# Kernel tuning notes

Measured on AMD Instinct MI355X. Metric: run time of the kernel, lower is better.

Reference implementation:

```python
import jax, jax.numpy as jnp
import numpy as np

N = 8192
D = 256
ALPHA = 0.2  # LeakyReLU negative slope
NEG_INF = -9e15


def setup_inputs() -> dict:
    key = jax.random.key(0)
    k1, k2, k3, k4, k5, k6 = jax.random.split(key, 6)
    inputs = jax.random.normal(k1, (N, D), dtype=jnp.float32)
    # sparse random binary adjacency, avg degree ~32, plus self loops
    adj = (jax.random.uniform(k2, (N, N)) < (32.0 / N)).astype(jnp.float32)
    adj = jnp.maximum(adj, jnp.eye(N, dtype=jnp.float32))
    cmt_weight = jax.random.uniform(k3, (N, 1), dtype=jnp.float32)  # unused by SPGAT
    W = jax.random.normal(k4, (D, D), dtype=jnp.float32) * (1.0 / np.sqrt(D))
    a1 = jax.random.normal(k5, (D, 1), dtype=jnp.float32) * 0.1
    a2 = jax.random.normal(k6, (D, 1), dtype=jnp.float32) * 0.1
    return {"inputs": inputs, "adj": adj, "cmt_weight": cmt_weight,
            "W": W, "a1": a1, "a2": a2}


def reference(inputs, adj, cmt_weight, W, a1, a2):
    # SPGAT (batched GAT layer with batch=1, squeezed):
    Wh = inputs @ W                       # [N, D]
    f1 = Wh @ a1                          # [N, 1]
    f2 = Wh @ a2                          # [N, 1]
    e = jax.nn.leaky_relu(f1 + f2.T, negative_slope=ALPHA)  # [N, N]
    scores = jnp.where(adj > 0, e, NEG_INF)
    att = jax.nn.softmax(scores, axis=-1)  # [N, N]
    node_out = jax.nn.relu(att @ Wh)       # [N, D]
    return node_out
```

## Files before the change

### kernel.cpp

```cpp
#include <hip/hip_runtime.h>
#include <hip/hip_bf16.h>
#include <math.h>

#define NN 8192
#define DD 256
#define DEG_CAP 128
constexpr float ALPHA = 0.2f;

typedef __attribute__((ext_vector_type(4))) float f32x4;
typedef __attribute__((ext_vector_type(8))) short bf16x8;
typedef __attribute__((ext_vector_type(8))) unsigned short u16x8;

__global__ __launch_bounds__(256) void k_convX(const float* __restrict__ X,
                                               short* __restrict__ Xhi,
                                               short* __restrict__ Xlo) {
    int i = blockIdx.x * 256 + threadIdx.x;
    float4 v = ((const float4*)X)[i];
    float f[4] = {v.x, v.y, v.z, v.w};
    short h[4], l[4];
    #pragma unroll
    for (int q = 0; q < 4; ++q) {
        __hip_bfloat16 hb = __float2bfloat16(f[q]);
        float hf = __bfloat162float(hb);
        __hip_bfloat16 lb = __float2bfloat16(f[q] - hf);
        h[q] = __builtin_bit_cast(short, hb);
        l[q] = __builtin_bit_cast(short, lb);
    }
    *(short4*)(Xhi + (size_t)i * 4) = make_short4(h[0], h[1], h[2], h[3]);
    *(short4*)(Xlo + (size_t)i * 4) = make_short4(l[0], l[1], l[2], l[3]);
}

__global__ __launch_bounds__(256) void k_convW(const float* __restrict__ W,
                                               short* __restrict__ WhiT,
                                               short* __restrict__ WloT) {
    __shared__ float tile[64][65];
    const int n0 = (blockIdx.x & 3) * 64;
    const int k0 = (blockIdx.x >> 2) * 64;
    const int c = threadIdx.x & 63;
    const int rg = threadIdx.x >> 6;
    #pragma unroll
    for (int i = 0; i < 16; ++i) {
        int r = rg * 16 + i;
        tile[r][c] = W[(size_t)(k0 + r) * DD + n0 + c];
    }
    __syncthreads();
    #pragma unroll
    for (int i = 0; i < 16; ++i) {
        int rw = rg * 16 + i;
        float x = tile[c][rw];
        __hip_bfloat16 hb = __float2bfloat16(x);
        float hf = __bfloat162float(hb);
        __hip_bfloat16 lb = __float2bfloat16(x - hf);
        WhiT[(size_t)(n0 + rw) * DD + k0 + c] = __builtin_bit_cast(short, hb);
        WloT[(size_t)(n0 + rw) * DD + k0 + c] = __builtin_bit_cast(short, lb);
    }
}

#define LDA 40
__global__ __launch_bounds__(256) void k_gemm(const short* __restrict__ Xhi,
                                              const short* __restrict__ Xlo,
                                              const short* __restrict__ WhiT,
                                              const short* __restrict__ WloT,
                                              float* __restrict__ Wh,
                                              unsigned short* __restrict__ Whb) {
    __shared__ short sAh[64 * LDA], sAl[64 * LDA];
    __shared__ short sBh[64 * LDA], sBl[64 * LDA];
    const int tid = threadIdx.x;
    const int lane = tid & 63;
    const int wid = tid >> 6;
    const int wm = wid >> 1, wn = wid & 1;
    const int row0 = (blockIdx.x >> 2) * 64;
    const int col0 = (blockIdx.x & 3) * 64;
    f32x4 acc[2][2] = {};
    for (int k0 = 0; k0 < DD; k0 += 32) {
        {
            int r = tid >> 2, sg = tid & 3;
            *(int4*)(sAh + r * LDA + sg * 8) =
                *(const int4*)(Xhi + (size_t)(row0 + r) * DD + k0 + sg * 8);
            *(int4*)(sAl + r * LDA + sg * 8) =
                *(const int4*)(Xlo + (size_t)(row0 + r) * DD + k0 + sg * 8);
            *(int4*)(sBh + r * LDA + sg * 8) =
                *(const int4*)(WhiT + (size_t)(col0 + r) * DD + k0 + sg * 8);
            *(int4*)(sBl + r * LDA + sg * 8) =
                *(const int4*)(WloT + (size_t)(col0 + r) * DD + k0 + sg * 8);
        }
        __syncthreads();
        const int kb = (lane >> 4) * 8;
        const int ar = wm * 32 + (lane & 15);
        const int br = wn * 32 + (lane & 15);
        bf16x8 ah[2], al[2], bh[2], bl[2];
        #pragma unroll
        for (int mi = 0; mi < 2; ++mi) {
            ah[mi] = *(const bf16x8*)(sAh + (ar + mi * 16) * LDA + kb);
            al[mi] = *(const bf16x8*)(sAl + (ar + mi * 16) * LDA + kb);
        }
        #pragma unroll
        for (int ni = 0; ni < 2; ++ni) {
            bh[ni] = *(const bf16x8*)(sBh + (br + ni * 16) * LDA + kb);
            bl[ni] = *(const bf16x8*)(sBl + (br + ni * 16) * LDA + kb);
        }
        #pragma unroll
        for (int mi = 0; mi < 2; ++mi)
            #pragma unroll
            for (int ni = 0; ni < 2; ++ni) {
                acc[mi][ni] = __builtin_amdgcn_mfma_f32_16x16x32_bf16(ah[mi], bh[ni], acc[mi][ni], 0, 0, 0);
                acc[mi][ni] = __builtin_amdgcn_mfma_f32_16x16x32_bf16(ah[mi], bl[ni], acc[mi][ni], 0, 0, 0);
                acc[mi][ni] = __builtin_amdgcn_mfma_f32_16x16x32_bf16(al[mi], bh[ni], acc[mi][ni], 0, 0, 0);
            }
        __syncthreads();
    }
    const int orow = row0 + wm * 32 + (lane >> 4) * 4;
    const int ocol = col0 + wn * 32 + (lane & 15);
    #pragma unroll
    for (int mi = 0; mi < 2; ++mi)
        #pragma unroll
        for (int ni = 0; ni < 2; ++ni)
            #pragma unroll
            for (int r = 0; r < 4; ++r) {
                float x = acc[mi][ni][r];
                size_t idx = (size_t)(orow + mi * 16 + r) * DD + ocol + ni * 16;
                Wh[idx] = x;
                Whb[idx] = __builtin_bit_cast(unsigned short, __float2bfloat16(x));
            }
}

__global__ __launch_bounds__(256) void k_f12(const float* __restrict__ Wh,
                                             const float* __restrict__ a1,
                                             const float* __restrict__ a2,
                                             float* __restrict__ f1,
                                             float* __restrict__ f2) {
    const int wid = threadIdx.x >> 6;
    const int lane = threadIdx.x & 63;
    const int row = blockIdx.x * 4 + wid;
    float4 w  = *(const float4*)(Wh + (size_t)row * DD + lane * 4);
    float4 v1 = *(const float4*)(a1 + lane * 4);
    float4 v2 = *(const float4*)(a2 + lane * 4);
    float s1 = w.x * v1.x + w.y * v1.y + w.z * v1.z + w.w * v1.w;
    float s2 = w.x * v2.x + w.y * v2.y + w.z * v2.z + w.w * v2.w;
    #pragma unroll
    for (int o = 32; o; o >>= 1) {
        s1 += __shfl_down(s1, o);
        s2 += __shfl_down(s2, o);
    }
    if (lane == 0) { f1[row] = s1; f2[row] = s2; }
}

__global__ __launch_bounds__(256) void k_gat6(const float* __restrict__ adj,
                                              const unsigned short* __restrict__ Whb,
                                              const float* __restrict__ f1,
                                              const float* __restrict__ f2,
                                              float* __restrict__ out) {
    __shared__ int   s_j[4][DEG_CAP];
    __shared__ float s_e[4][DEG_CAP];
    const int tid = threadIdx.x;
    const int lane = tid & 63, wid = tid >> 6;
    const int row = blockIdx.x * 4 + wid;
    s_e[wid][lane]      = -INFINITY;
    s_e[wid][lane + 64] = -INFINITY;
    const float f1i = f1[row];
    const f32x4* arow = (const f32x4*)(adj + (size_t)row * NN);
    int base = 0;
    for (int ch = 0; ch < 8; ++ch) {
        f32x4 v[4];
        #pragma unroll
        for (int u = 0; u < 4; ++u)
            v[u] = __builtin_nontemporal_load(&arow[ch * 256 + u * 64 + lane]);
        #pragma unroll
        for (int u = 0; u < 4; ++u) {
            #pragma unroll
            for (int q = 0; q < 4; ++q) {
                bool hit = v[u][q] > 0.f;
                unsigned long long mask = __ballot(hit);
                if (hit) {
                    int pos = base + __popcll(mask & ((1ull << lane) - 1ull));
                    if (pos < DEG_CAP) {
                        int j = (ch * 256 + u * 64 + lane) * 4 + q;
                        float e = f1i + f2[j];
                        e = e > 0.f ? e : ALPHA * e;
                        s_j[wid][pos] = j;
                        s_e[wid][pos] = e;
                    }
                }
                base += __popcll(mask);
            }
        }
    }
    const int cw = base < DEG_CAP ? base : DEG_CAP;
    float e0 = s_e[wid][lane], e1 = s_e[wid][lane + 64];
    float mx = fmaxf(e0, e1);
    #pragma unroll
    for (int o = 32; o; o >>= 1) mx = fmaxf(mx, __shfl_xor(mx, o));
    float sm = __expf(e0 - mx) + __expf(e1 - mx);
    #pragma unroll
    for (int o = 32; o; o >>= 1) sm += __shfl_xor(sm, o);
    const int half = lane >> 5, sl = lane & 31;
    const int* sj = s_j[wid];
    const float* se = s_e[wid];
    f32x4 accA = {0.f, 0.f, 0.f, 0.f};
    f32x4 accB = {0.f, 0.f, 0.f, 0.f};
    {
        auto ld = [&](int kk) -> u16x8 {
            int idx = kk + half;
            int j = sj[idx < cw ? idx : 0];
            return *(const u16x8*)(Whb + (size_t)j * DD + sl * 8);
        };
        u16x8 b0 = ld(0), b1 = ld(2), b2 = ld(4), b3 = ld(6);
        for (int kk = 0; kk < cw; kk += 8) {
            #pragma unroll
            for (int p = 0; p < 4; ++p) {
                u16x8 cur = p == 0 ? b0 : p == 1 ? b1 : p == 2 ? b2 : b3;
                int idx = kk + p * 2 + half;
                float w = idx < cw ? __expf(se[idx] - mx) : 0.f;
                #pragma unroll
                for (int q = 0; q < 4; ++q) {
                    float lo = __builtin_bit_cast(float, (unsigned)cur[2 * q] << 16);
                    float hi = __builtin_bit_cast(float, (unsigned)cur[2 * q + 1] << 16);
                    if (q < 2) {
                        accA[2 * q]     = fmaf(w, lo, accA[2 * q]);
                        accA[2 * q + 1] = fmaf(w, hi, accA[2 * q + 1]);
                    } else {
                        accB[2 * (q - 2)]     = fmaf(w, lo, accB[2 * (q - 2)]);
                        accB[2 * (q - 2) + 1] = fmaf(w, hi, accB[2 * (q - 2) + 1]);
                    }
                }
            }
            b0 = ld(kk + 8); b1 = ld(kk + 10); b2 = ld(kk + 12); b3 = ld(kk + 14);
        }
    }
    #pragma unroll
    for (int q = 0; q < 4; ++q) {
        accA[q] += __shfl_xor(accA[q], 32);
        accB[q] += __shfl_xor(accB[q], 32);
    }
    const float inv = 1.f / sm;
    if (half == 0) {
        f32x4 r0, r1;
        #pragma unroll
        for (int q = 0; q < 4; ++q) {
            float oa = accA[q] * inv, ob = accB[q] * inv;
            r0[q] = oa > 0.f ? oa : 0.f;
            r1[q] = ob > 0.f ? ob : 0.f;
        }
        float* op = out + (size_t)row * DD + sl * 8;
        __builtin_nontemporal_store(r0, (f32x4*)op);
        __builtin_nontemporal_store(r1, (f32x4*)(op + 4));
    }
}

extern "C" void kernel_launch(void* const* d_in, const int* in_sizes, int n_in,
                              void* d_out, int out_size, void* d_ws, size_t ws_size,
                              hipStream_t stream) {
    const float* X   = (const float*)d_in[0];
    const float* adj = (const float*)d_in[1];
    const float* W   = (const float*)d_in[3];
    const float* a1  = (const float*)d_in[4];
    const float* a2  = (const float*)d_in[5];
    float* out = (float*)d_out;

    short* Xhi  = (short*)d_ws;
    short* Xlo  = Xhi + (size_t)NN * DD;
    short* WhiT = Xlo + (size_t)NN * DD;
    short* WloT = WhiT + (size_t)DD * DD;
    float* Wh   = (float*)(WloT + (size_t)DD * DD);
    float* f1   = Wh + (size_t)NN * DD;
    float* f2   = f1 + NN;
    unsigned short* Whb = (unsigned short*)(f2 + NN);

    k_convX<<<(NN * DD / 4) / 256, 256, 0, stream>>>(X, Xhi, Xlo);
    k_convW<<<16, 256, 0, stream>>>(W, WhiT, WloT);
    k_gemm<<<(NN / 64) * (DD / 64), 256, 0, stream>>>(Xhi, Xlo, WhiT, WloT, Wh, Whb);
    k_f12<<<NN / 4, 256, 0, stream>>>(Wh, a1, a2, f1, f2);
    k_gat6<<<NN / 4, 256, 0, stream>>>(adj, Whb, f1, f2, out);
}
```

Before: 82.94 us.

## Fuse X split conversion and f1/f2 projection into a full-width GEMM

Removes the separate X hi/lo conversion kernel and the f1/f2 dot-product kernel. The GEMM now reads fp32 X directly, splits it to bf16 hi/lo in shared memory, and computes a full 256-column row tile per block so it can reduce Wh·a1 and Wh·a2 in the epilogue. It no longer writes the fp32 Wh buffer. This cuts global traffic and launches, but each block now reloads the whole W^T slice per k-step and uses more LDS, which may lower occupancy.

```diff
diff --git a/kernel.cpp b/kernel.cpp
--- a/kernel.cpp
+++ b/kernel.cpp
@@ -10,25 +10,6 @@
 typedef __attribute__((ext_vector_type(4))) float f32x4;
 typedef __attribute__((ext_vector_type(8))) short bf16x8;
 typedef __attribute__((ext_vector_type(8))) unsigned short u16x8;
-
-__global__ __launch_bounds__(256) void k_convX(const float* __restrict__ X,
-                                               short* __restrict__ Xhi,
-                                               short* __restrict__ Xlo) {
-    int i = blockIdx.x * 256 + threadIdx.x;
-    float4 v = ((const float4*)X)[i];
-    float f[4] = {v.x, v.y, v.z, v.w};
-    short h[4], l[4];
-    #pragma unroll
-    for (int q = 0; q < 4; ++q) {
-        __hip_bfloat16 hb = __float2bfloat16(f[q]);
-        float hf = __bfloat162float(hb);
-        __hip_bfloat16 lb = __float2bfloat16(f[q] - hf);
-        h[q] = __builtin_bit_cast(short, hb);
-        l[q] = __builtin_bit_cast(short, lb);
-    }
-    *(short4*)(Xhi + (size_t)i * 4) = make_short4(h[0], h[1], h[2], h[3]);
-    *(short4*)(Xlo + (size_t)i * 4) = make_short4(l[0], l[1], l[2], l[3]);
-}
 
 __global__ __launch_bounds__(256) void k_convW(const float* __restrict__ W,
                                                short* __restrict__ WhiT,
@@ -56,93 +37,103 @@
     }
 }
 
-#define LDA 40
-__global__ __launch_bounds__(256) void k_gemm(const short* __restrict__ Xhi,
-                                              const short* __restrict__ Xlo,
-                                              const short* __restrict__ WhiT,
-                                              const short* __restrict__ WloT,
-                                              float* __restrict__ Wh,
-                                              unsigned short* __restrict__ Whb) {
-    __shared__ short sAh[64 * LDA], sAl[64 * LDA];
-    __shared__ short sBh[64 * LDA], sBl[64 * LDA];
+#define LDAx 40
+__global__ __launch_bounds__(256) void k_gemm2(const float* __restrict__ X,
+                                               const short* __restrict__ WhiT,
+                                               const short* __restrict__ WloT,
+                                               const float* __restrict__ a1,
+                                               const float* __restrict__ a2,
+                                               unsigned short* __restrict__ Whb,
+                                               float* __restrict__ f1,
+                                               float* __restrict__ f2) {
+    __shared__ short sAh[32 * LDAx], sAl[32 * LDAx];
+    __shared__ short sBh[256 * LDAx], sBl[256 * LDAx];
+    __shared__ float sP[2][2][32];
     const int tid = threadIdx.x;
     const int lane = tid & 63;
     const int wid = tid >> 6;
     const int wm = wid >> 1, wn = wid & 1;
-    const int row0 = (blockIdx.x >> 2) * 64;
-    const int col0 = (blockIdx.x & 3) * 64;
-    f32x4 acc[2][2] = {};
+    const int row0 = blockIdx.x * 32;
+    f32x4 acc[4][2] = {};
     for (int k0 = 0; k0 < DD; k0 += 32) {
         {
-            int r = tid >> 2, sg = tid & 3;
-            *(int4*)(sAh + r * LDA + sg * 8) =
-                *(const int4*)(Xhi + (size_t)(row0 + r) * DD + k0 + sg * 8);
-            *(int4*)(sAl + r * LDA + sg * 8) =
-                *(const int4*)(Xlo + (size_t)(row0 + r) * DD + k0 + sg * 8);
-            *(int4*)(sBh + r * LDA + sg * 8) =
-                *(const int4*)(WhiT + (size_t)(col0 + r) * DD + k0 + sg * 8);
-            *(int4*)(sBl + r * LDA + sg * 8) =
-                *(const int4*)(WloT + (size_t)(col0 + r) * DD + k0 + sg * 8);
+            int r = tid >> 3, c4 = tid & 7;
+            f32x4 xv = *(const f32x4*)(X + (size_t)(row0 + r) * DD + k0 + c4 * 4);
+            short hx[4], lx[4];
+            #pragma unroll
+            for (int q = 0; q < 4; ++q) {
+                __hip_bfloat16 hb = __float2bfloat16(xv[q]);
+                float hf = __bfloat162float(hb);
+                __hip_bfloat16 lb = __float2bfloat16(xv[q] - hf);
+                hx[q] = __builtin_bit_cast(short, hb);
+                lx[q] = __builtin_bit_cast(short, lb);
+            }
+            *(short4*)(sAh + r * LDAx + c4 * 4) = make_short4(hx[0], hx[1], hx[2], hx[3]);
+            *(short4*)(sAl + r * LDAx + c4 * 4) = make_short4(lx[0], lx[1], lx[2], lx[3]);
+            const int4* srcH = (const int4*)(WhiT + (size_t)tid * DD + k0);
+            const int4* srcL = (const int4*)(WloT + (size_t)tid * DD + k0);
+            #pragma unroll
+            for (int j = 0; j < 4; ++j) {
+                *(int4*)(sBh + tid * LDAx + j * 8) = srcH[j];
+                *(int4*)(sBl + tid * LDAx + j * 8) = srcL[j];
+            }
         }
         __syncthreads();
         const int kb = (lane >> 4) * 8;
-        const int ar = wm * 32 + (lane & 15);
-        const int br = wn * 32 + (lane & 15);
-        bf16x8 ah[2], al[2], bh[2], bl[2];
-        #pragma unroll
-        for (int mi = 0; mi < 2; ++mi) {
-            ah[mi] = *(const bf16x8*)(sAh + (ar + mi * 16) * LDA + kb);
-            al[mi] = *(const bf16x8*)(sAl + (ar + mi * 16) * LDA + kb);
-        }
+        const int l15 = lane & 15;
+        bf16x8 ah = *(const bf16x8*)(sAh + (wm * 16 + l15) * LDAx + kb);
+        bf16x8 al = *(const bf16x8*)(sAl + (wm * 16 + l15) * LDAx + kb);
+        #pragma unroll
+        for (int ct = 0; ct < 4; ++ct)
+            #pragma unroll
+            for (int ni = 0; ni < 2; ++ni) {
+                int br = ct * 64 + wn * 32 + ni * 16 + l15;
+                bf16x8 bh = *(const bf16x8*)(sBh + br * LDAx + kb);
+                bf16x8 bl = *(const bf16x8*)(sBl + br * LDAx + kb);
+                acc[ct][ni] = __builtin_amdgcn_mfma_f32_16x16x32_bf16(ah, bh, acc[ct][ni], 0, 0, 0);
+                acc[ct][ni] = __builtin_amdgcn_mfma_f32_16x16x32_bf16(ah, bl, acc[ct][ni], 0, 0, 0);
+                acc[ct][ni] = __builtin_amdgcn_mfma_f32_16x16x32_bf16(al, bh, acc[ct][ni], 0, 0, 0);
+            }
+        __syncthreads();
+    }
+    const int l15 = lane & 15;
+    const int orow = row0 + wm * 16 + (lane >> 4) * 4;
+    float s1[4] = {0.f, 0.f, 0.f, 0.f}, s2[4] = {0.f, 0.f, 0.f, 0.f};
+    #pragma unroll
+    for (int ct = 0; ct < 4; ++ct)
         #pragma unroll
         for (int ni = 0; ni < 2; ++ni) {
-            bh[ni] = *(const bf16x8*)(sBh + (br + ni * 16) * LDA + kb);
-            bl[ni] = *(const bf16x8*)(sBl + (br + ni * 16) * LDA + kb);
-        }
-        #pragma unroll
-        for (int mi = 0; mi < 2; ++mi)
-            #pragma unroll
-            for (int ni = 0; ni < 2; ++ni) {
-                acc[mi][ni] = __builtin_amdgcn_mfma_f32_16x16x32_bf16(ah[mi], bh[ni], acc[mi][ni], 0, 0, 0);
-                acc[mi][ni] = __builtin_amdgcn_mfma_f32_16x16x32_bf16(ah[mi], bl[ni], acc[mi][ni], 0, 0, 0);
-                acc[mi][ni] = __builtin_amdgcn_mfma_f32_16x16x32_bf16(al[mi], bh[ni], acc[mi][ni], 0, 0, 0);
-            }
-        __syncthreads();
-    }
-    const int orow = row0 + wm * 32 + (lane >> 4) * 4;
-    const int ocol = col0 + wn * 32 + (lane & 15);
-    #pragma unroll
-    for (int mi = 0; mi < 2; ++mi)
-        #pragma unroll
-        for (int ni = 0; ni < 2; ++ni)
+            int cc = ct * 64 + wn * 32 + ni * 16 + l15;
+            float A1 = a1[cc], A2 = a2[cc];
             #pragma unroll
             for (int r = 0; r < 4; ++r) {
-                float x = acc[mi][ni][r];
-                size_t idx = (size_t)(orow + mi * 16 + r) * DD + ocol + ni * 16;
-                Wh[idx] = x;
-                Whb[idx] = __builtin_bit_cast(unsigned short, __float2bfloat16(x));
-            }
-}
-
-__global__ __launch_bounds__(256) void k_f12(const float* __restrict__ Wh,
-                                             const float* __restrict__ a1,
-                                             const float* __restrict__ a2,
-                                             float* __restrict__ f1,
-                                             float* __restrict__ f2) {
-    const int wid = threadIdx.x >> 6;
-    const int lane = threadIdx.x & 63;
-    const int row = blockIdx.x * 4 + wid;
-    float4 w  = *(const float4*)(Wh + (size_t)row * DD + lane * 4);
-    float4 v1 = *(const float4*)(a1 + lane * 4);
-    float4 v2 = *(const float4*)(a2 + lane * 4);
-    float s1 = w.x * v1.x + w.y * v1.y + w.z * v1.z + w.w * v1.w;
-    float s2 = w.x * v2.x + w.y * v2.y + w.z * v2.z + w.w * v2.w;
-    #pragma unroll
-    for (int o = 32; o; o >>= 1) {
-        s1 += __shfl_down(s1, o);
-        s2 += __shfl_down(s2, o);
-    }
-    if (lane == 0) { f1[row] = s1; f2[row] = s2; }
+                float x = acc[ct][ni][r];
+                Whb[(size_t)(orow + r) * DD + cc] =
+                    __builtin_bit_cast(unsigned short, __float2bfloat16(x));
+                s1[r] = fmaf(x, A1, s1[r]);
+                s2[r] = fmaf(x, A2, s2[r]);
+            }
+        }
+    #pragma unroll
+    for (int o = 1; o < 16; o <<= 1)
+        #pragma unroll
+        for (int r = 0; r < 4; ++r) {
+            s1[r] += __shfl_xor(s1[r], o);
+            s2[r] += __shfl_xor(s2[r], o);
+        }
+    if (l15 == 0) {
+        #pragma unroll
+        for (int r = 0; r < 4; ++r) {
+            int lr = wm * 16 + (lane >> 4) * 4 + r;
+            sP[0][wn][lr] = s1[r];
+            sP[1][wn][lr] = s2[r];
+        }
+    }
+    __syncthreads();
+    if (tid < 32) {
+        f1[row0 + tid] = sP[0][0][tid] + sP[0][1][tid];
+        f2[row0 + tid] = sP[1][0][tid] + sP[1][1][tid];
+    }
 }
 
 __global__ __launch_bounds__(256) void k_gat6(const float* __restrict__ adj,
@@ -257,18 +248,13 @@
     const float* a2  = (const float*)d_in[5];
     float* out = (float*)d_out;
 
-    short* Xhi  = (short*)d_ws;
-    short* Xlo  = Xhi + (size_t)NN * DD;
-    short* WhiT = Xlo + (size_t)NN * DD;
+    short* WhiT = (short*)d_ws;
     short* WloT = WhiT + (size_t)DD * DD;
-    float* Wh   = (float*)(WloT + (size_t)DD * DD);
-    float* f1   = Wh + (size_t)NN * DD;
+    float* f1   = (float*)(WloT + (size_t)DD * DD);
     float* f2   = f1 + NN;
     unsigned short* Whb = (unsigned short*)(f2 + NN);
 
-    k_convX<<<(NN * DD / 4) / 256, 256, 0, stream>>>(X, Xhi, Xlo);
     k_convW<<<16, 256, 0, stream>>>(W, WhiT, WloT);
-    k_gemm<<<(NN / 64) * (DD / 64), 256, 0, stream>>>(Xhi, Xlo, WhiT, WloT, Wh, Whb);
-    k_f12<<<NN / 4, 256, 0, stream>>>(Wh, a1, a2, f1, f2);
+    k_gemm2<<<NN / 32, 256, 0, stream>>>(X, WhiT, WloT, a1, a2, Whb, f1, f2);
     k_gat6<<<NN / 4, 256, 0, stream>>>(adj, Whb, f1, f2, out);
 }
```

After: 86.33 us. 4.1% more time.
